# Performance work log

Hardware: AMD Instinct MI355X
Metric: run time of the kernel (lower is better)

Reference implementation:

```python
import jax, jax.numpy as jnp
import numpy as np

DIM = 4096  # N must equal dim for the elementwise atten * v broadcast


def setup_inputs() -> dict:
    key = jax.random.key(0)
    ks = jax.random.split(key, 7)
    s = 1.0 / np.sqrt(DIM)  # keep Linear-like magnitudes
    return {
        "x": jax.random.normal(ks[0], (DIM, DIM), dtype=jnp.float32),
        "Wq": jax.random.normal(ks[1], (DIM, DIM), dtype=jnp.float32) * s,
        "bq": jax.random.normal(ks[2], (DIM,), dtype=jnp.float32) * s,
        "Wk": jax.random.normal(ks[3], (DIM, DIM), dtype=jnp.float32) * s,
        "bk": jax.random.normal(ks[4], (DIM,), dtype=jnp.float32) * s,
        "Wv": jax.random.normal(ks[5], (DIM, DIM), dtype=jnp.float32) * s,
        "bv": jax.random.normal(ks[6], (DIM,), dtype=jnp.float32) * s,
    }


def reference(x, Wq, bq, Wk, bk, Wv, bv):
    # torch nn.Linear: y = x @ W.T + b
    scale = x.shape[-1] ** -0.5
    q = x @ Wq.T + bq                      # [N, d]
    k = x @ Wk.T + bk                      # [N, d]
    v = x @ Wv.T + bv                      # [N, d]
    atten = jnp.einsum("nd,md->nm", q, k) * scale  # [N, N]
    atten = jax.nn.softmax(atten, axis=-1)
    return atten * v                       # elementwise (N == d)
```

## Files before the change

### kernel.cpp

```cpp
#include <hip/hip_runtime.h>
#include <cstdint>
#include <cstddef>


#define NDIM 4096

typedef __bf16 bf16x8 __attribute__((ext_vector_type(8)));
typedef float f32x4 __attribute__((ext_vector_type(4)));
typedef unsigned short us8 __attribute__((ext_vector_type(8)));

__device__ __forceinline__ unsigned short f2bf(float f) {
  unsigned int u = __float_as_uint(f);
  return (unsigned short)((u + 0x7fffu + ((u >> 16) & 1u)) >> 16);
}

__device__ __forceinline__ void async_copy16(void* lds, const void* g) {
  __builtin_amdgcn_global_load_lds(
      (__attribute__((address_space(1))) void*)(uintptr_t)g,
      (__attribute__((address_space(3))) void*)lds,
      16, 0, 0);
}

__global__ __launch_bounds__(256) void cvt2_f32_to_bf16(
    const float* __restrict__ s0, unsigned short* __restrict__ d0,
    const float* __restrict__ s1, unsigned short* __restrict__ d1) {
  const float* src = blockIdx.y ? s1 : s0;
  unsigned short* dst = blockIdx.y ? d1 : d0;
  const int i = blockIdx.x * 256 + threadIdx.x;
  const float4* s = (const float4*)src;
  float4 a = s[2 * i];
  float4 b = s[2 * i + 1];
  us8 o;
  o[0] = f2bf(a.x); o[1] = f2bf(a.y); o[2] = f2bf(a.z); o[3] = f2bf(a.w);
  o[4] = f2bf(b.x); o[5] = f2bf(b.y); o[6] = f2bf(b.z); o[7] = f2bf(b.w);
  ((us8*)dst)[i] = o;
}


#define STG4A(Ao, Bo, kn)                                        \
  async_copy16((Ao) + t * 8,          Asrc + (kn));              \
  async_copy16((Ao) + 8192 + t * 8,   Asrc + (kn) + 524288);     \
  async_copy16((Bo) + t * 8,          Bsrc + (kn));              \
  async_copy16((Bo) + 4096 + t * 8,   Bsrc + (kn) + 262144);

#define STG4B(Ao, Bo, kn)                                        \
  async_copy16((Ao) + 4096 + t * 8,   Asrc + (kn) + 262144);     \
  async_copy16((Ao) + 12288 + t * 8,  Asrc + (kn) + 786432);     \
  async_copy16((Bo) + 8192 + t * 8,   Bsrc + (kn) + 524288);     \
  async_copy16((Bo) + 12288 + t * 8,  Bsrc + (kn) + 786432);

#define RDA(Ac, ROFF)                                                          \
  _Pragma("unroll") for (int i = 0; i < 4; ++i) {                              \
    a[i][0] = *(const bf16x8*)((const char*)(Ac) + (aob + ((ROFF) + i) * 2048));        \
    a[i][1] = *(const bf16x8*)((const char*)(Ac) + ((aob + ((ROFF) + i) * 2048) ^ 64)); \
  }

#define RDB(Bc, J0)                                                            \
  _Pragma("unroll") for (int jj = 0; jj < 2; ++jj) {                           \
    b[(J0) + jj][0] = *(const bf16x8*)((const char*)(Bc) + (bob + ((J0) + jj) * 2048));        \
    b[(J0) + jj][1] = *(const bf16x8*)((const char*)(Bc) + ((bob + ((J0) + jj) * 2048) ^ 64)); \
  }

#define MFMA16(IO, J0)                                                         \
  _Pragma("unroll") for (int i = 0; i < 4; ++i)                                \
  _Pragma("unroll") for (int jj = 0; jj < 2; ++jj)                             \
  _Pragma("unroll") for (int ks = 0; ks < 2; ++ks)                             \
    acc[(IO) + i][(J0) + jj] = __builtin_amdgcn_mfma_f32_16x16x32_bf16(        \
        a[i][ks], b[(J0) + jj][ks], acc[(IO) + i][(J0) + jj], 0, 0, 0);

#define KTILE(Ac, Bc, Ao, Bo, kn, VM, DOSTAGE)                                 \
  {                                                                            \
    if (DOSTAGE) { STG4A(Ao, Bo, kn) }                                         \
    asm volatile("s_waitcnt vmcnt(" #VM ")" ::: "memory");                     \
    __builtin_amdgcn_s_barrier();                                              \
    __builtin_amdgcn_sched_barrier(0);                                         \
    RDA(Ac, 0)                                                                 \
    RDB(Bc, 0)                                                                 \
    if (DOSTAGE) { STG4B(Ao, Bo, kn) }                                         \
    __builtin_amdgcn_s_barrier();                                              \
    __builtin_amdgcn_sched_barrier(0);                                         \
    __builtin_amdgcn_s_setprio(1);                                             \
    MFMA16(0, 0)                                                               \
    __builtin_amdgcn_s_setprio(0);                                             \
    __builtin_amdgcn_s_barrier();                                              \
    __builtin_amdgcn_sched_barrier(0);                                         \
    RDB(Bc, 2)                                                                 \
    __builtin_amdgcn_s_barrier();                                              \
    __builtin_amdgcn_sched_barrier(0);                                         \
    __builtin_amdgcn_s_setprio(1);                                             \
    MFMA16(0, 2)                                                               \
    __builtin_amdgcn_s_setprio(0);                                             \
    __builtin_amdgcn_s_barrier();                                              \
    __builtin_amdgcn_sched_barrier(0);                                         \
    RDA(Ac, 4)                                                                 \
    __builtin_amdgcn_s_barrier();                                              \
    __builtin_amdgcn_sched_barrier(0);                                         \
    __builtin_amdgcn_s_setprio(1);                                             \
    MFMA16(4, 2)                                                               \
    __builtin_amdgcn_s_setprio(0);                                             \
    __builtin_amdgcn_s_barrier();                                              \
    __builtin_amdgcn_sched_barrier(0);                                         \
    __builtin_amdgcn_s_setprio(1);                                             \
    MFMA16(4, 0)                                                               \
    __builtin_amdgcn_s_setprio(0);                                             \
  }

__device__ __forceinline__ void gemm_core256(
    const unsigned short* __restrict__ A, const unsigned short* __restrict__ B,
    int bm, int bn, int t, unsigned short* LDS ,
    f32x4 acc[8][4]) {
  const int wave = t >> 6, lane = t & 63;
  const int wm = wave >> 2, wn = wave & 3;
  const int quad = lane >> 4, l16 = lane & 15;

  unsigned short* A0 = LDS;
  unsigned short* B0 = LDS + 16384;
  unsigned short* A1 = LDS + 32768;
  unsigned short* B1 = LDS + 49152;

  const int srow = t >> 3;
  const int scol = ((t ^ (t >> 3)) & 7) * 8;
  const unsigned short* Asrc = A + (size_t)(bm * 256 + srow) * NDIM + scol;
  const unsigned short* Bsrc = B + (size_t)(bn * 256 + srow) * NDIM + scol;

  const int colx = (quad * 16) ^ ((l16 & 7) << 4);
  const int aob = wm * 16384 + l16 * 128 + colx;
  const int bob = wn * 8192 + l16 * 128 + colx;

  bf16x8 a[4][2], b[4][2];

#pragma unroll
  for (int c = 0; c < 4; ++c) {
    async_copy16(A0 + c * 4096 + t * 8, Asrc + (size_t)c * 262144);
    async_copy16(B0 + c * 4096 + t * 8, Bsrc + (size_t)c * 262144);
  }

#pragma unroll 1
  for (int kt = 0; kt < 31; ++kt) {
    const size_t kA = (size_t)(2 * kt + 1) * 64;
    KTILE(A0, B0, A1, B1, kA, 4, true)
    const size_t kB = (size_t)(2 * kt + 2) * 64;
    KTILE(A1, B1, A0, B0, kB, 4, true)
  }
  KTILE(A0, B0, A1, B1, (size_t)4032, 4, true)
  KTILE(A1, B1, A0, B0, (size_t)0, 0, false)
}

#undef KTILE
#undef MFMA16
#undef RDA
#undef RDB
#undef STG4A
#undef STG4B

__global__ __launch_bounds__(512, 2) void gemm_qkv(
    const unsigned short* __restrict__ A,
    const unsigned short* __restrict__ B0,
    const unsigned short* __restrict__ B1,
    const unsigned short* __restrict__ B2,
    const float* __restrict__ bias0, const float* __restrict__ bias1,
    const float* __restrict__ bias2,
    unsigned short* __restrict__ qo, unsigned short* __restrict__ ko,
    float* __restrict__ vo) {
  __shared__ __align__(1024) unsigned short LDS[65536];

  const int t = threadIdx.x;
  const int bm = blockIdx.y, bn = blockIdx.x, z = blockIdx.z;
  const unsigned short* B = (z == 0) ? B0 : (z == 1) ? B1 : B2;
  const float* bias = (z == 0) ? bias0 : (z == 1) ? bias1 : bias2;

  const f32x4 zero = {0.f, 0.f, 0.f, 0.f};
  f32x4 acc[8][4];
#pragma unroll
  for (int i = 0; i < 8; ++i)
#pragma unroll
    for (int j = 0; j < 4; ++j) acc[i][j] = zero;

  gemm_core256(A, B, bm, bn, t, LDS, acc);

  const int wave = t >> 6, lane = t & 63;
  const int wm = wave >> 2, wn = wave & 3;
  const int quad = lane >> 4, l16 = lane & 15;
  unsigned short* ob = (z == 1) ? ko : qo;
#pragma unroll
  for (int j = 0; j < 4; ++j) {
    const int col = bn * 256 + wn * 64 + j * 16 + l16;
    const float bb = bias[col];
#pragma unroll
    for (int i = 0; i < 8; ++i) {
      const int row0 = bm * 256 + wm * 128 + i * 16 + quad * 4;
#pragma unroll
      for (int r = 0; r < 4; ++r) {
        const size_t idx = (size_t)(row0 + r) * NDIM + col;
        const float val = acc[i][j][r] + bb;
        if (z == 2) vo[idx] = val;
        else        ob[idx] = f2bf(val);
      }
    }
  }
}

__global__ __launch_bounds__(512, 2) void gemm_s(
    const unsigned short* __restrict__ A, const unsigned short* __restrict__ B,
    float* __restrict__ C, float scale) {
  __shared__ __align__(1024) unsigned short LDS[65536];

  const int t = threadIdx.x;
  const int bm = blockIdx.y, bn = blockIdx.x;

  const f32x4 zero = {0.f, 0.f, 0.f, 0.f};
  f32x4 acc[8][4];
#pragma unroll
  for (int i = 0; i < 8; ++i)
#pragma unroll
    for (int j = 0; j < 4; ++j) acc[i][j] = zero;

  gemm_core256(A, B, bm, bn, t, LDS, acc);

  const int wave = t >> 6, lane = t & 63;
  const int wm = wave >> 2, wn = wave & 3;
  const int quad = lane >> 4, l16 = lane & 15;
#pragma unroll
  for (int j = 0; j < 4; ++j) {
    const int col = bn * 256 + wn * 64 + j * 16 + l16;
#pragma unroll
    for (int i = 0; i < 8; ++i) {
      const int row0 = bm * 256 + wm * 128 + i * 16 + quad * 4;
#pragma unroll
      for (int r = 0; r < 4; ++r)
        C[(size_t)(row0 + r) * NDIM + col] = acc[i][j][r] * scale;
    }
  }
}

__global__ __launch_bounds__(256) void softmax_mul(
    const float* __restrict__ S, const float* __restrict__ V,
    float* __restrict__ out) {
  const int row = blockIdx.x;
  const int t = threadIdx.x;
  const int lane = t & 63, wave = t >> 6;
  const float4* Sr = (const float4*)(S + (size_t)row * NDIM);
  const float4* Vr = (const float4*)(V + (size_t)row * NDIM);
  float4* Or = (float4*)(out + (size_t)row * NDIM);

  float4 p[4];
  float m = -3.4e38f;
#pragma unroll
  for (int c = 0; c < 4; ++c) {
    p[c] = Sr[t + 256 * c];
    m = fmaxf(m, fmaxf(fmaxf(p[c].x, p[c].y), fmaxf(p[c].z, p[c].w)));
  }
#pragma unroll
  for (int off = 32; off > 0; off >>= 1) m = fmaxf(m, __shfl_xor(m, off));
  __shared__ float redm[4], reds[4];
  if (lane == 0) redm[wave] = m;
  __syncthreads();
  m = fmaxf(fmaxf(redm[0], redm[1]), fmaxf(redm[2], redm[3]));

  float s = 0.f;
#pragma unroll
  for (int c = 0; c < 4; ++c) {
    p[c].x = __expf(p[c].x - m);
    p[c].y = __expf(p[c].y - m);
    p[c].z = __expf(p[c].z - m);
    p[c].w = __expf(p[c].w - m);
    s += (p[c].x + p[c].y) + (p[c].z + p[c].w);
  }
#pragma unroll
  for (int off = 32; off > 0; off >>= 1) s += __shfl_xor(s, off);
  if (lane == 0) reds[wave] = s;
  __syncthreads();
  s = (reds[0] + reds[1]) + (reds[2] + reds[3]);
  const float inv = 1.0f / s;

#pragma unroll
  for (int c = 0; c < 4; ++c) {
    float4 vv = Vr[t + 256 * c];
    float4 o;
    o.x = p[c].x * inv * vv.x;
    o.y = p[c].y * inv * vv.y;
    o.z = p[c].z * inv * vv.z;
    o.w = p[c].w * inv * vv.w;
    Or[t + 256 * c] = o;
  }
}

extern "C" void kernel_launch(void* const* d_in, const int* in_sizes, int n_in,
                              void* d_out, int out_size, void* d_ws, size_t ws_size,
                              hipStream_t stream) {
  const float* x  = (const float*)d_in[0];
  const float* Wq = (const float*)d_in[1];
  const float* bq = (const float*)d_in[2];
  const float* Wk = (const float*)d_in[3];
  const float* bk = (const float*)d_in[4];
  const float* Wv = (const float*)d_in[5];
  const float* bv = (const float*)d_in[6];
  float* out = (float*)d_out;

  const size_t NN = (size_t)NDIM * NDIM;

  unsigned short* xb  = (unsigned short*)d_out;
  unsigned short* wqb = xb + NN;
  unsigned short* wkb = (unsigned short*)d_in[1];
  unsigned short* wvb = wkb + NN;
  unsigned short* qb  = (unsigned short*)d_in[3];
  unsigned short* kb  = qb + NN;
  float*          vf  = (float*)d_in[5];
  float*          Sf  = (float*)d_out;

  const int cvtBlocks = (int)(NN / (256 * 8));

  cvt2_f32_to_bf16<<<dim3(cvtBlocks, 2), 256, 0, stream>>>(x, xb, Wq, wqb);
  cvt2_f32_to_bf16<<<dim3(cvtBlocks, 2), 256, 0, stream>>>(Wk, wkb, Wv, wvb);

  gemm_qkv<<<dim3(16, 16, 3), 512, 0, stream>>>(xb, wqb, wkb, wvb,
                                                bq, bk, bv, qb, kb, vf);

  gemm_s<<<dim3(16, 16), 512, 0, stream>>>(qb, kb, Sf, 0.015625f);

  softmax_mul<<<NDIM, 256, 0, stream>>>(Sf, vf, out);
}
```

Baseline: 736.8 us.

## Simplify GEMM k-loop to single-barrier double buffering without ping-pong barriers

Replaces the barrier-interleaved ping-pong schedule in the QKV GEMM core with a plain double-buffered loop. Each k-tile now waits for all outstanding loads, takes one barrier, issues all eight async copies for the next tile, then runs its LDS reads and MFMAs with no further barriers. The aim is to cut barrier and synchronisation overhead. In exchange it gives up the staggered wave scheduling that overlapped LDS reads with other waves' MFMA work, and the full vmcnt(0) wait can expose global-load latency.

Result: faster. 718.0 us (-2.6%).

```diff
diff --git a/kernel.cpp b/kernel.cpp
--- a/kernel.cpp
+++ b/kernel.cpp
@@ -37,15 +37,13 @@
 }
 
 
-#define STG4A(Ao, Bo, kn)                                        \
+#define STG8(Ao, Bo, kn)                                         \
   async_copy16((Ao) + t * 8,          Asrc + (kn));              \
+  async_copy16((Ao) + 4096 + t * 8,   Asrc + (kn) + 262144);     \
   async_copy16((Ao) + 8192 + t * 8,   Asrc + (kn) + 524288);     \
+  async_copy16((Ao) + 12288 + t * 8,  Asrc + (kn) + 786432);     \
   async_copy16((Bo) + t * 8,          Bsrc + (kn));              \
-  async_copy16((Bo) + 4096 + t * 8,   Bsrc + (kn) + 262144);
-
-#define STG4B(Ao, Bo, kn)                                        \
-  async_copy16((Ao) + 4096 + t * 8,   Asrc + (kn) + 262144);     \
-  async_copy16((Ao) + 12288 + t * 8,  Asrc + (kn) + 786432);     \
+  async_copy16((Bo) + 4096 + t * 8,   Bsrc + (kn) + 262144);     \
   async_copy16((Bo) + 8192 + t * 8,   Bsrc + (kn) + 524288);     \
   async_copy16((Bo) + 12288 + t * 8,  Bsrc + (kn) + 786432);
 
@@ -68,39 +66,24 @@
     acc[(IO) + i][(J0) + jj] = __builtin_amdgcn_mfma_f32_16x16x32_bf16(        \
         a[i][ks], b[(J0) + jj][ks], acc[(IO) + i][(J0) + jj], 0, 0, 0);
 
-#define KTILE(Ac, Bc, Ao, Bo, kn, VM, DOSTAGE)                                 \
+#define KTILE(Ac, Bc, Ao, Bo, kn, DOSTAGE)                                     \
   {                                                                            \
-    if (DOSTAGE) { STG4A(Ao, Bo, kn) }                                         \
-    asm volatile("s_waitcnt vmcnt(" #VM ")" ::: "memory");                     \
+    asm volatile("s_waitcnt vmcnt(0)" ::: "memory");                           \
     __builtin_amdgcn_s_barrier();                                              \
     __builtin_amdgcn_sched_barrier(0);                                         \
+    if (DOSTAGE) { STG8(Ao, Bo, kn) }                                          \
     RDA(Ac, 0)                                                                 \
     RDB(Bc, 0)                                                                 \
-    if (DOSTAGE) { STG4B(Ao, Bo, kn) }                                         \
-    __builtin_amdgcn_s_barrier();                                              \
-    __builtin_amdgcn_sched_barrier(0);                                         \
     __builtin_amdgcn_s_setprio(1);                                             \
     MFMA16(0, 0)                                                               \
     __builtin_amdgcn_s_setprio(0);                                             \
-    __builtin_amdgcn_s_barrier();                                              \
-    __builtin_amdgcn_sched_barrier(0);                                         \
     RDB(Bc, 2)                                                                 \
-    __builtin_amdgcn_s_barrier();                                              \
-    __builtin_amdgcn_sched_barrier(0);                                         \
     __builtin_amdgcn_s_setprio(1);                                             \
     MFMA16(0, 2)                                                               \
     __builtin_amdgcn_s_setprio(0);                                             \
-    __builtin_amdgcn_s_barrier();                                              \
-    __builtin_amdgcn_sched_barrier(0);                                         \
     RDA(Ac, 4)                                                                 \
-    __builtin_amdgcn_s_barrier();                                              \
-    __builtin_amdgcn_sched_barrier(0);                                         \
     __builtin_amdgcn_s_setprio(1);                                             \
     MFMA16(4, 2)                                                               \
-    __builtin_amdgcn_s_setprio(0);                                             \
-    __builtin_amdgcn_s_barrier();                                              \
-    __builtin_amdgcn_sched_barrier(0);                                         \
-    __builtin_amdgcn_s_setprio(1);                                             \
     MFMA16(4, 0)                                                               \
     __builtin_amdgcn_s_setprio(0);                                             \
   }
@@ -138,20 +121,19 @@
 #pragma unroll 1
   for (int kt = 0; kt < 31; ++kt) {
     const size_t kA = (size_t)(2 * kt + 1) * 64;
-    KTILE(A0, B0, A1, B1, kA, 4, true)
+    KTILE(A0, B0, A1, B1, kA, true)
     const size_t kB = (size_t)(2 * kt + 2) * 64;
-    KTILE(A1, B1, A0, B0, kB, 4, true)
-  }
-  KTILE(A0, B0, A1, B1, (size_t)4032, 4, true)
-  KTILE(A1, B1, A0, B0, (size_t)0, 0, false)
+    KTILE(A1, B1, A0, B0, kB, true)
+  }
+  KTILE(A0, B0, A1, B1, (size_t)4032, true)
+  KTILE(A1, B1, A0, B0, (size_t)0, false)
 }
 
 #undef KTILE
 #undef MFMA16
 #undef RDA
 #undef RDB
-#undef STG4A
-#undef STG4B
+#undef STG8
 
 __global__ __launch_bounds__(512, 2) void gemm_qkv(
     const unsigned short* __restrict__ A,
```
